# Kernel tuning notes

Hardware: AMD Instinct MI355X
Metric: run time of the kernel (lower is better)

The kernel has to match this reference:

```python
import jax, jax.numpy as jnp
import numpy as np
from jax import lax

V, E, H, M, B, L = 4000, 256, 256, 128, 32, 4
PUNC, ENG, NUM, EOS = 0, 1, 2, 3
LOGINF = 1000000.0


def _lstm(xs, h0, c0, Wih, Whh, bih, bhh):
    # xs: [T, N, H]; single-layer torch LSTM, gate order i,f,g,o
    def step(carry, x):
        h, c = carry
        g = x @ Wih.T + bih + h @ Whh.T + bhh
        i, f, gg, o = jnp.split(g, 4, axis=-1)
        c = jax.nn.sigmoid(f) * c + jax.nn.sigmoid(i) * jnp.tanh(gg)
        h = jax.nn.sigmoid(o) * jnp.tanh(c)
        return (h, c), h
    _, hs = lax.scan(step, (h0, c0), xs)
    return hs


def _forward(x, lengths, embedding, e2v_b, enc_Wih, enc_Whh, enc_bih, enc_bhh,
             enc_h0, enc_c0, dec_Wih, dec_Whh, dec_bih, dec_bhh,
             dht_W, dht_b, sos_W, sos_b):
    xT = x.T  # [M, B]
    inputs = embedding[xT]  # [M, B, H]
    is_single = ((xT == PUNC) | (xT == ENG) | (xT == NUM)).astype(jnp.float32) * (-LOGINF)  # [M, B]

    # context encoder (learned init states broadcast over batch), output halved
    h0 = jnp.broadcast_to(enc_h0, (B, H))
    c0 = jnp.broadcast_to(enc_c0, (B, H))
    enc_out = _lstm(inputs, h0, c0, enc_Wih, enc_Whh, enc_bih, enc_bhh) * 0.5  # [M, B, H]

    S = M - 2
    starts = jnp.arange(1, M - 1)  # [S] segment start positions
    enc_prev = enc_out[starts - 1]  # [S, B, H]
    sos = enc_prev @ sos_W.T + sos_b                       # start-of-segment symbol [S,B,H]
    dec_h0 = jnp.tanh(enc_prev @ dht_W.T + dht_b)          # decoder h init (1 layer) [S,B,H]
    dec_c0 = jnp.zeros_like(dec_h0)

    pad_in = jnp.concatenate([inputs, jnp.zeros((L, B, H), inputs.dtype)], axis=0)  # [M+L,B,H]
    idx = starts[:, None] + jnp.arange(L)[None, :]  # [S, L] token positions j_start+t
    seg_in = pad_in[idx]  # [S, L, B, H]
    dec_in = jnp.concatenate([sos[:, None], seg_in], axis=1)  # [S, L+1, B, H]
    dec_in = dec_in.transpose(1, 0, 2, 3).reshape(L + 1, S * B, H)
    dec_out = _lstm(dec_in, dec_h0.reshape(S * B, H), dec_c0.reshape(S * B, H),
                    dec_Wih, dec_Whh, dec_bih, dec_bhh).reshape(L + 1, S, B, H)

    logits = jnp.einsum('tsbh,vh->tsbv', dec_out, embedding) + e2v_b  # tied e2v weight
    logp = jax.nn.log_softmax(logits, axis=-1)  # [L+1, S, B, V]

    x_pad = jnp.concatenate([xT, jnp.zeros((L, B), xT.dtype)], axis=0)
    tgt = x_pad[idx]  # [S, L, B]
    lp_t = logp[:L].transpose(1, 0, 2, 3)  # [S, L, B, V]
    tlp = jnp.take_along_axis(lp_t, tgt[..., None].astype(jnp.int32), axis=-1)[..., 0]  # [S,L,B]

    is_pad = jnp.concatenate([is_single, jnp.zeros((L, B), jnp.float32)], axis=0)
    seg_is = is_pad[idx]  # is_single[j_start+t], [S,L,B]
    kge1 = (jnp.arange(L) >= 1).astype(jnp.float32)[None, :, None]  # t>=1 mask
    cum = jnp.cumsum(tlp + seg_is * kge1, axis=1)
    cum = cum + kge1 * is_single[starts][:, None, :]  # add is_single[j_start] once from k==1 on

    eos_lp = logp[1:, :, :, EOS].transpose(1, 0, 2)  # [S, L, B]
    logpy_seg = cum + eos_lp
    j_len = jnp.minimum(L, (M - 1) - starts)  # [S]
    kvalid = jnp.arange(L)[None, :] < j_len[:, None]
    logpy_seg = jnp.where(kvalid[:, :, None], logpy_seg, -LOGINF)

    row0 = jnp.full((1, L, B), -LOGINF, jnp.float32).at[0, 0].set(0.0)
    logpy = jnp.concatenate([row0, logpy_seg], axis=0)  # [M-1, L, B]

    # seg_lp[e, d-1] = logpy[j_start+1 = e-(d-1)][d-1] for segment length d ending at e
    e_idx = jnp.arange(M - 1)[:, None] - jnp.arange(L)[None, :]  # [M-1, L]
    gathered = logpy[jnp.clip(e_idx, 0, M - 2), jnp.arange(L)[None, :]]  # [M-1, L, B]
    seg_lp = jnp.where((e_idx >= 1)[:, :, None], gathered, -LOGINF)

    def dp_step(buf, lp_e):  # buf[d-1] = alpha[e-d], [L, B]
        a = jax.scipy.special.logsumexp(buf + lp_e, axis=0)  # [B]
        return jnp.concatenate([a[None], buf[:-1]], axis=0), a

    buf0 = jnp.full((L, B), -LOGINF, jnp.float32).at[0].set(0.0)  # alpha[0]=0
    _, alphas_rest = lax.scan(dp_step, buf0, seg_lp[1:])  # e = 1..M-2
    alphas = jnp.concatenate([jnp.zeros((1, B), jnp.float32), alphas_rest], axis=0)  # [M-1, B]

    nll = -alphas[lengths - 2, jnp.arange(B)]
    total = jnp.sum(lengths) - 2 * B
    return jnp.sum(nll) / total.astype(jnp.float32)


def setup_inputs() -> dict:
    key = jax.random.key(0)
    ks = jax.random.split(key, 16)
    w = lambda k, shape: (jax.random.normal(k, shape, jnp.float32) * 0.05)
    return {
        'x': jax.random.randint(ks[0], (B, M), 0, V, jnp.int32),
        'lengths': jnp.full((B,), M, jnp.int32),
        'embedding': jax.random.uniform(ks[1], (V, E), jnp.float32, -1.0, 1.0),
        'e2v_b': w(ks[2], (V,)),
        'enc_Wih': w(ks[3], (4 * H, H)),
        'enc_Whh': w(ks[4], (4 * H, H)),
        'enc_bih': w(ks[5], (4 * H,)),
        'enc_bhh': w(ks[6], (4 * H,)),
        'enc_h0': jnp.zeros((1, H), jnp.float32),
        'enc_c0': jnp.zeros((1, H), jnp.float32),
        'dec_Wih': w(ks[7], (4 * H, H)),
        'dec_Whh': w(ks[8], (4 * H, H)),
        'dec_bih': w(ks[9], (4 * H,)),
        'dec_bhh': w(ks[10], (4 * H,)),
        'dht_W': w(ks[11], (H, H)),
        'dht_b': w(ks[12], (H,)),
        'sos_W': w(ks[13], (H, H)),
        'sos_b': w(ks[14], (H,)),
    }


def reference(x, lengths, embedding, e2v_b, enc_Wih, enc_Whh, enc_bih, enc_bhh,
              enc_h0, enc_c0, dec_Wih, dec_Whh, dec_bih, dec_bhh,
              dht_W, dht_b, sos_W, sos_b):
    return _forward(x, lengths, embedding, e2v_b, enc_Wih, enc_Whh, enc_bih, enc_bhh,
                    enc_h0, enc_c0, dec_Wih, dec_Whh, dec_bih, dec_bhh,
                    dht_W, dht_b, sos_W, sos_b)
```

## Files before the change

kernel.cpp:

```cpp
#include <hip/hip_runtime.h>
#include <math.h>


#define LOGNEG -1000000.0f
#define GF_BIAS 1
#define GF_TANH 2
#define GF_F16OUT 16
#define ZSHIFT 8.0f

typedef unsigned int uint32;
typedef _Float16 half2_t __attribute__((ext_vector_type(2)));
typedef _Float16 half8_t __attribute__((ext_vector_type(8)));
typedef float    f32x4_t __attribute__((ext_vector_type(4)));

__device__ __forceinline__ float sigmf_(float x){ return 1.0f/(1.0f+expf(-x)); }

__device__ __forceinline__ float dot2f(uint32 w, uint32 h, float acc){
#if __has_builtin(__builtin_amdgcn_fdot2)
    return __builtin_amdgcn_fdot2(__builtin_bit_cast(half2_t, w),
                                  __builtin_bit_cast(half2_t, h), acc, false);
#else
    half2_t a = __builtin_bit_cast(half2_t, w);
    half2_t b = __builtin_bit_cast(half2_t, h);
    return acc + (float)a[0]*(float)b[0] + (float)a[1]*(float)b[1];
#endif
}

__device__ __forceinline__ void gemm16_body(
    _Float16* Bs, int tid,
    const _Float16* __restrict__ A, const _Float16* __restrict__ W,
    const float* __restrict__ bias, float* __restrict__ C,
    _Float16* __restrict__ C16, int N, int flags, int rowBlk, int colBlk)
{
    int wave = tid >> 6, lane = tid & 63;
    int ln = lane & 15, quad = lane >> 4;
    half8_t a[8];
    if (tid < 256){
        #pragma unroll
        for (int i = 0; i < 8; i++){
            int idx = i*256 + tid;
            int row = idx >> 5, c16 = idx & 31;
            *(uint4*)&Bs[row*264 + c16*8] =
                *(const uint4*)(W + (size_t)(colBlk+row)*256 + c16*8);
        }
        const half8_t* Ap = (const half8_t*)(A + (size_t)(rowBlk + wave*16 + ln)*256 + quad*8);
        #pragma unroll
        for (int ks = 0; ks < 8; ks++) a[ks] = Ap[ks*4];
    }
    __syncthreads();
    if (tid < 256){
        #pragma unroll
        for (int ct = 0; ct < 4; ct++){
            f32x4_t c4 = {0.f,0.f,0.f,0.f};
            const _Float16* bp = &Bs[(ct*16+ln)*264 + quad*8];
            #pragma unroll
            for (int ks = 0; ks < 8; ks++){
                half8_t b = *(const half8_t*)(bp + ks*32);
                c4 = __builtin_amdgcn_mfma_f32_16x16x32_f16(a[ks], b, c4, 0, 0, 0);
            }
            int c = colBlk + ct*16 + ln;
            #pragma unroll
            for (int reg = 0; reg < 4; reg++){
                int r = rowBlk + wave*16 + quad*4 + reg;
                float v = c4[reg];
                if (flags & GF_BIAS) v += bias[c];
                if (flags & GF_TANH) v = tanhf(v);
                if (flags & GF_F16OUT) C16[(size_t)r*N + c] = (_Float16)v;
                else                   C  [(size_t)r*N + c] = v;
            }
        }
    }
}

__global__ __launch_bounds__(256) void k_prep(
    const int* __restrict__ x,
    const float* __restrict__ emb, const float* __restrict__ e2v_b,
    const float* __restrict__ eWih, const float* __restrict__ dWih,
    const float* __restrict__ dWhh, const float* __restrict__ eWhh,
    const float* __restrict__ sosW, const float* __restrict__ dhtW,
    const float* __restrict__ ebih, const float* __restrict__ ebhh,
    const float* __restrict__ dbih, const float* __restrict__ dbhh,
    _Float16* __restrict__ emb16, float* __restrict__ biasOff,
    _Float16* __restrict__ dWih16, _Float16* __restrict__ dWhh16,
    _Float16* __restrict__ eWhh16, _Float16* __restrict__ sosW16,
    _Float16* __restrict__ dhtW16, float* __restrict__ bias_d,
    _Float16* __restrict__ emb_in16, float* __restrict__ is_s,
    _Float16* __restrict__ XgE16)
{
    __shared__ _Float16 Bs[64*264];
    int bx = blockIdx.x, tid = threadIdx.x;
    if (bx < 1465){
        #pragma unroll 1
        for (int rr = 0; rr < 8; rr++){
            int v = bx*8 + rr;
            if (v >= 11716) break;
            if (v < 4032){
                int row = v;
                emb16[(size_t)row*256 + tid] = (row < 4000) ? (_Float16)emb[(size_t)row*256 + tid] : (_Float16)0.0f;
                if (tid == 0) biasOff[row] = (row < 4000) ? (e2v_b[row] - ZSHIFT) : -200.0f;
            } else if (v < 5056){
                int r = v - 4032; dWih16[(size_t)r*256 + tid] = (_Float16)dWih[(size_t)r*256 + tid];
            } else if (v < 6080){
                int r = v - 5056; dWhh16[(size_t)r*256 + tid] = (_Float16)dWhh[(size_t)r*256 + tid];
            } else if (v < 7104){
                int r = v - 6080; eWhh16[(size_t)r*256 + tid] = (_Float16)eWhh[(size_t)r*256 + tid];
            } else if (v < 7360){
                int r = v - 7104; sosW16[(size_t)r*256 + tid] = (_Float16)sosW[(size_t)r*256 + tid];
            } else if (v < 7616){
                int r = v - 7360; dhtW16[(size_t)r*256 + tid] = (_Float16)dhtW[(size_t)r*256 + tid];
            } else if (v < 7620){
                int j = (v - 7616)*256 + tid;
                if (j < 1024) bias_d[j] = dbih[j] + dbhh[j];
            } else {
                int ri = v - 7620;
                int m = ri >> 5, b = ri & 31;
                int tok = x[b*128 + m];
                emb_in16[(size_t)ri*256 + tid] = (_Float16)emb[(size_t)tok*256 + tid];
                if (tid == 0) is_s[ri] = (tok <= 2) ? LOGNEG : 0.0f;
            }
        }
    } else {
        int tile = bx - 1465;
        int rowBlk = (tile >> 4)*64, colBlk = (tile & 15)*64;
        #pragma unroll
        for (int i = 0; i < 8; i++){
            int idx = i*256 + tid;
            int row = idx >> 5, c16 = idx & 31;
            const float* src = eWih + (size_t)(colBlk+row)*256 + c16*8;
            float4 f0 = *(const float4*)src;
            float4 f1 = *(const float4*)(src + 4);
            half8_t hv;
            hv[0]=(_Float16)f0.x; hv[1]=(_Float16)f0.y; hv[2]=(_Float16)f0.z; hv[3]=(_Float16)f0.w;
            hv[4]=(_Float16)f1.x; hv[5]=(_Float16)f1.y; hv[6]=(_Float16)f1.z; hv[7]=(_Float16)f1.w;
            *(half8_t*)&Bs[row*264 + c16*8] = hv;
        }
        int wave = tid >> 6, lane = tid & 63;
        int ln = lane & 15, quad = lane >> 4;
        int r = rowBlk + wave*16 + ln;
        int m = r >> 5, b_ = r & 31;
        int tok = x[b_*128 + m];
        half8_t a[8];
        #pragma unroll
        for (int ks = 0; ks < 8; ks++){
            const float* ap = emb + (size_t)tok*256 + quad*8 + ks*32;
            float4 f0 = *(const float4*)ap;
            float4 f1 = *(const float4*)(ap + 4);
            half8_t hv;
            hv[0]=(_Float16)f0.x; hv[1]=(_Float16)f0.y; hv[2]=(_Float16)f0.z; hv[3]=(_Float16)f0.w;
            hv[4]=(_Float16)f1.x; hv[5]=(_Float16)f1.y; hv[6]=(_Float16)f1.z; hv[7]=(_Float16)f1.w;
            a[ks] = hv;
        }
        __syncthreads();
        #pragma unroll
        for (int ct = 0; ct < 4; ct++){
            f32x4_t c4 = {0.f,0.f,0.f,0.f};
            const _Float16* bp = &Bs[(ct*16+ln)*264 + quad*8];
            #pragma unroll
            for (int ks = 0; ks < 8; ks++){
                half8_t b = *(const half8_t*)(bp + ks*32);
                c4 = __builtin_amdgcn_mfma_f32_16x16x32_f16(a[ks], b, c4, 0, 0, 0);
            }
            int c = colBlk + ct*16 + ln;
            float bb = ebih[c] + ebhh[c];
            #pragma unroll
            for (int reg = 0; reg < 4; reg++){
                int rr2 = rowBlk + wave*16 + quad*4 + reg;
                XgE16[(size_t)rr2*1024 + c] = (_Float16)(c4[reg] + bb);
            }
        }
    }
}

__global__ void __attribute__((amdgpu_flat_work_group_size(512,512), amdgpu_waves_per_eu(2,2)))
k_enc_rnn(
    const _Float16* __restrict__ Xg16, const _Float16* __restrict__ Whh16,
    const float* __restrict__ h0, const float* __restrict__ c0,
    _Float16* __restrict__ enc_out16,
    const _Float16* __restrict__ emb_in16, const _Float16* __restrict__ dWih16,
    const float* __restrict__ bias_d, _Float16* __restrict__ Xg16dec)
{
    extern __shared__ char smem[];
    const int bx = blockIdx.x, tid = threadIdx.x;
    if (bx >= 32){
        int eng = tid >> 8, ltid = tid & 255;
        _Float16* Bs = (_Float16*)smem + (size_t)eng*(64*264);
        int base = (bx - 32)*2 + eng;
        for (int rnd = 0; rnd < 3; rnd++){
            int tile = rnd*448 + base;
            __syncthreads();
            if (tile < 1024)
                gemm16_body(Bs, ltid, emb_in16, dWih16, bias_d, nullptr, Xg16dec,
                            1024, GF_BIAS|GF_F16OUT, (tile >> 4)*64, (tile & 15)*64);
            else
                __syncthreads();
        }
        return;
    }
    uint4*     wlds = (uint4*)smem;
    _Float16*  hb   = (_Float16*)(smem + 147456);
    const int b = bx;
    const int w_ = tid >> 6, l_ = tid & 63;
    const int u  = w_*32 + (l_ & 31);
    const int hi = l_ >> 5;
    const int rA = hi*512 + u;
    const int rB = rA + 256;

    const uint4* pA = (const uint4*)(Whh16 + (size_t)rA*256);
    const uint4* pB = (const uint4*)(Whh16 + (size_t)rB*256);
    uint4 wA[23], wB[23];
    #pragma unroll
    for (int i = 0; i < 23; i++){ wA[i] = pA[i]; wB[i] = pB[i]; }
    #pragma unroll
    for (int i = 0; i < 9; i++){
        wlds[(i*2 + 0)*512 + tid] = pA[23 + i];
        wlds[(i*2 + 1)*512 + tid] = pB[23 + i];
    }
    float c = c0[u];
    if (tid < 256) hb[tid] = (_Float16)h0[tid];
    __syncthreads();

    float xgA = (float)Xg16[(size_t)b*1024 + rA];
    float xgB = (float)Xg16[(size_t)b*1024 + rB];

    for (int t = 0; t < 128; t++){
        const int cur = t & 1, nxt = cur ^ 1;
        float nxgA = 0.f, nxgB = 0.f;
        if (t < 127){
            const _Float16* xp = Xg16 + ((size_t)((t+1)*32 + b))*1024;
            nxgA = (float)xp[rA]; nxgB = (float)xp[rB];
        }
        const uint4* hu4 = (const uint4*)(hb + cur*256);
        float aA = 0.f, aB = 0.f;
        #pragma unroll
        for (int i = 0; i < 23; i++){
            uint4 hh = hu4[i];
            aA = dot2f(wA[i].x, hh.x, aA); aA = dot2f(wA[i].y, hh.y, aA);
            aA = dot2f(wA[i].z, hh.z, aA); aA = dot2f(wA[i].w, hh.w, aA);
            aB = dot2f(wB[i].x, hh.x, aB); aB = dot2f(wB[i].y, hh.y, aB);
            aB = dot2f(wB[i].z, hh.z, aB); aB = dot2f(wB[i].w, hh.w, aB);
        }
        #pragma unroll
        for (int i = 0; i < 9; i++){
            uint4 hh = hu4[23 + i];
            uint4 vA = wlds[(i*2 + 0)*512 + tid];
            uint4 vB = wlds[(i*2 + 1)*512 + tid];
            aA = dot2f(vA.x, hh.x, aA); aA = dot2f(vA.y, hh.y, aA);
            aA = dot2f(vA.z, hh.z, aA); aA = dot2f(vA.w, hh.w, aA);
            aB = dot2f(vB.x, hh.x, aB); aB = dot2f(vB.y, hh.y, aB);
            aB = dot2f(vB.z, hh.z, aB); aB = dot2f(vB.w, hh.w, aB);
        }
        float gA = aA + xgA, gB = aB + xgB;
        float oA = __shfl_xor(gA, 32, 64);
        float oB = __shfl_xor(gB, 32, 64);
        float gi = hi ? oA : gA;
        float gf = hi ? oB : gB;
        float gg = hi ? gA : oA;
        float go = hi ? gB : oB;
        c = sigmf_(gf)*c + sigmf_(gi)*tanhf(gg);
        float hn = sigmf_(go)*tanhf(c);
        if (!hi){
            enc_out16[((size_t)(t*32 + b))*256 + u] = (_Float16)(0.5f*hn);
            hb[nxt*256 + u] = (_Float16)hn;
        }
        __syncthreads();
        xgA = nxgA; xgB = nxgB;
    }
}

__global__ __launch_bounds__(256) void k_head(
    const _Float16* __restrict__ enc_out16,
    const _Float16* __restrict__ sosW16, const float* __restrict__ sos_b, _Float16* __restrict__ sos16,
    const _Float16* __restrict__ dhtW16, const float* __restrict__ dht_b, _Float16* __restrict__ dech0_16)
{
    __shared__ _Float16 Bs[64*264];
    int z = blockIdx.z;
    gemm16_body(Bs, threadIdx.x, enc_out16,
                z ? dhtW16 : sosW16, z ? dht_b : sos_b, nullptr,
                z ? dech0_16 : sos16, 256,
                z ? (GF_BIAS|GF_TANH|GF_F16OUT) : (GF_BIAS|GF_F16OUT),
                blockIdx.y*64, blockIdx.x*64);
}

__global__ __launch_bounds__(256) void k_dec_step(
    const _Float16* __restrict__ hprev, const _Float16* __restrict__ sosA,
    const _Float16* __restrict__ dWhh16, const _Float16* __restrict__ dWih16,
    const _Float16* __restrict__ base16, const float* __restrict__ bias_d,
    float* __restrict__ dec_c, _Float16* __restrict__ dec16_j, int jstep)
{
    __shared__ _Float16 Bs[64*264];
    int tid = threadIdx.x;
    int wave = tid >> 6, lane = tid & 63;
    int ln = lane & 15, quad = lane >> 4;
    int u0 = blockIdx.x * 64, r0 = blockIdx.y * 64;

    half8_t aH[8], aS[8];
    {
        const half8_t* Ap = (const half8_t*)(hprev + (size_t)(r0 + wave*16 + ln)*256 + quad*8);
        #pragma unroll
        for (int ks = 0; ks < 8; ks++) aH[ks] = Ap[ks*4];
    }
    if (jstep == 0){
        const half8_t* Ap = (const half8_t*)(sosA + (size_t)(r0 + wave*16 + ln)*256 + quad*8);
        #pragma unroll
        for (int ks = 0; ks < 8; ks++) aS[ks] = Ap[ks*4];
    }

    f32x4_t cg[4][4];
    #pragma unroll
    for (int g = 0; g < 4; g++){
        int colBlk = g*256 + u0;
        __syncthreads();
        #pragma unroll
        for (int i = 0; i < 8; i++){
            int idx = i*256 + tid;
            int row = idx >> 5, c16 = idx & 31;
            *(uint4*)&Bs[row*264 + c16*8] =
                *(const uint4*)(dWhh16 + (size_t)(colBlk+row)*256 + c16*8);
        }
        __syncthreads();
        #pragma unroll
        for (int ct = 0; ct < 4; ct++){
            f32x4_t c4 = {0.f,0.f,0.f,0.f};
            const _Float16* bp = &Bs[(ct*16+ln)*264 + quad*8];
            #pragma unroll
            for (int ks = 0; ks < 8; ks++){
                half8_t b = *(const half8_t*)(bp + ks*32);
                c4 = __builtin_amdgcn_mfma_f32_16x16x32_f16(aH[ks], b, c4, 0, 0, 0);
            }
            cg[g][ct] = c4;
        }
        if (jstep == 0){
            __syncthreads();
            #pragma unroll
            for (int i = 0; i < 8; i++){
                int idx = i*256 + tid;
                int row = idx >> 5, c16 = idx & 31;
                *(uint4*)&Bs[row*264 + c16*8] =
                    *(const uint4*)(dWih16 + (size_t)(colBlk+row)*256 + c16*8);
            }
            __syncthreads();
            #pragma unroll
            for (int ct = 0; ct < 4; ct++){
                f32x4_t c4 = cg[g][ct];
                const _Float16* bp = &Bs[(ct*16+ln)*264 + quad*8];
                #pragma unroll
                for (int ks = 0; ks < 8; ks++){
                    half8_t b = *(const half8_t*)(bp + ks*32);
                    c4 = __builtin_amdgcn_mfma_f32_16x16x32_f16(aS[ks], b, c4, 0, 0, 0);
                }
                cg[g][ct] = c4;
            }
        }
    }
    #pragma unroll
    for (int ct = 0; ct < 4; ct++){
        int u = u0 + ct*16 + ln;
        #pragma unroll
        for (int reg = 0; reg < 4; reg++){
            int r = r0 + wave*16 + quad*4 + reg;
            float bi, bf, bg, bo;
            if (jstep == 0){
                bi = bias_d[u]; bf = bias_d[256+u]; bg = bias_d[512+u]; bo = bias_d[768+u];
            } else {
                int s = r >> 5, b_ = r & 31;
                int m = s + jstep;
                if (m < 128){
                    const _Float16* bp2 = base16 + (size_t)(m*32+b_)*1024 + u;
                    bi = (float)bp2[0]; bf = (float)bp2[256]; bg = (float)bp2[512]; bo = (float)bp2[768];
                } else {
                    bi = bias_d[u]; bf = bias_d[256+u]; bg = bias_d[512+u]; bo = bias_d[768+u];
                }
            }
            float gi = cg[0][ct][reg] + bi;
            float gf = cg[1][ct][reg] + bf;
            float gg = cg[2][ct][reg] + bg;
            float go = cg[3][ct][reg] + bo;
            float cv = (jstep == 0) ? 0.0f : dec_c[(size_t)r*256 + u];
            cv = sigmf_(gf)*cv + sigmf_(gi)*tanhf(gg);
            float hv = sigmf_(go)*tanhf(cv);
            dec_c[(size_t)r*256 + u] = cv;
            dec16_j[(size_t)r*256 + u] = (_Float16)hv;
        }
    }
}

__global__ __launch_bounds__(256) void k_logits(
    const _Float16* __restrict__ dec16, const _Float16* __restrict__ emb16,
    const float* __restrict__ biasOff, const int* __restrict__ x,
    float* __restrict__ ps, float* __restrict__ pzt, float* __restrict__ pze)
{
    __shared__ _Float16 Bs[64*264];
    __shared__ int tgt_s[128];
    int tid = threadIdx.x;
    int wave = tid >> 6, lane = tid & 63;
    int ln = lane & 15, quad = lane >> 4;
    int r0 = blockIdx.x * 128;
    int q = blockIdx.y;
    int vt0 = q*16, vt1 = (q == 3) ? 63 : (vt0 + 16);

    if (tid < 128){
        int r = r0 + tid;
        if (r >= 20160) r = 20159;
        int t = r / 4032, sb = r % 4032;
        int s_ = sb >> 5, b = sb & 31;
        int m = s_ + 1 + t;
        tgt_s[tid] = (m < 128) ? x[b*128 + m] : 0;
    }
    half8_t aA[8], aB[8];
    {
        int ra = r0 + wave*16 + ln;        if (ra >= 20160) ra = 20159;
        int rb = r0 + 64 + wave*16 + ln;   if (rb >= 20160) rb = 20159;
        const half8_t* Ap = (const half8_t*)(dec16 + (size_t)ra*256 + quad*8);
        const half8_t* Bp = (const half8_t*)(dec16 + (size_t)rb*256 + quad*8);
        #pragma unroll
        for (int ks = 0; ks < 8; ks++){ aA[ks] = Ap[ks*4]; aB[ks] = Bp[ks*4]; }
    }
    __syncthreads();
    int tgA[4], tgB[4];
    #pragma unroll
    for (int reg = 0; reg < 4; reg++){
        tgA[reg] = tgt_s[wave*16 + quad*4 + reg];
        tgB[reg] = tgt_s[64 + wave*16 + quad*4 + reg];
    }

    float sA[4] = {0.f,0.f,0.f,0.f}, sB[4] = {0.f,0.f,0.f,0.f};
    float ztA[4] = {-1e30f,-1e30f,-1e30f,-1e30f}, ztB[4] = {-1e30f,-1e30f,-1e30f,-1e30f};
    float zeA[4] = {-1e30f,-1e30f,-1e30f,-1e30f}, zeB[4] = {-1e30f,-1e30f,-1e30f,-1e30f};

    for (int vt = vt0; vt < vt1; vt++){
        int v0 = vt*64;
        __syncthreads();
        #pragma unroll
        for (int i = 0; i < 8; i++){
            int idx = i*256 + tid;
            int row = idx >> 5, c16 = idx & 31;
            *(uint4*)&Bs[row*264 + c16*8] =
                *(const uint4*)(emb16 + (size_t)(v0+row)*256 + c16*8);
        }
        __syncthreads();

        #pragma unroll
        for (int ct = 0; ct < 4; ct++){
            f32x4_t cA = {0.f,0.f,0.f,0.f}, cB = {0.f,0.f,0.f,0.f};
            const _Float16* bp = &Bs[(ct*16+ln)*264 + quad*8];
            #pragma unroll
            for (int ks = 0; ks < 8; ks++){
                half8_t b = *(const half8_t*)(bp + ks*32);
                cA = __builtin_amdgcn_mfma_f32_16x16x32_f16(aA[ks], b, cA, 0, 0, 0);
                cB = __builtin_amdgcn_mfma_f32_16x16x32_f16(aB[ks], b, cB, 0, 0, 0);
            }
            int vv = v0 + ct*16 + ln;
            float bb = biasOff[vv];
            #pragma unroll
            for (int reg = 0; reg < 4; reg++){
                float zA = cA[reg] + bb, zB = cB[reg] + bb;
                sA[reg] += __expf(zA);
                sB[reg] += __expf(zB);
                if (vv == tgA[reg]) ztA[reg] = zA;
                if (vv == tgB[reg]) ztB[reg] = zB;
                if (vv == 3){ zeA[reg] = zA; zeB[reg] = zB; }
            }
        }
    }
    #pragma unroll
    for (int reg = 0; reg < 4; reg++){
        float vsA = sA[reg], vtA = ztA[reg], veA = zeA[reg];
        float vsB = sB[reg], vtB = ztB[reg], veB = zeB[reg];
        #pragma unroll
        for (int off = 1; off < 16; off <<= 1){
            vsA += __shfl_xor(vsA, off, 64);
            vsB += __shfl_xor(vsB, off, 64);
            vtA = fmaxf(vtA, __shfl_xor(vtA, off, 64));
            vtB = fmaxf(vtB, __shfl_xor(vtB, off, 64));
            veA = fmaxf(veA, __shfl_xor(veA, off, 64));
            veB = fmaxf(veB, __shfl_xor(veB, off, 64));
        }
        if (ln == 0){
            int rA = r0 + wave*16 + quad*4 + reg;
            int rB = rA + 64;
            if (rA < 20160){ ps[q*20160+rA] = vsA; pzt[q*20160+rA] = vtA; pze[q*20160+rA] = veA; }
            if (rB < 20160){ ps[q*20160+rB] = vsB; pzt[q*20160+rB] = vtB; pze[q*20160+rB] = veB; }
        }
    }
}

__global__ __launch_bounds__(256) void k_comb_fin(
    const float* __restrict__ ps, const float* __restrict__ pzt,
    const float* __restrict__ pze, const int* __restrict__ x,
    const float* __restrict__ is_s, const int* __restrict__ lengths,
    float* __restrict__ tlp, float* __restrict__ eosb,
    float* __restrict__ seg_g, float* __restrict__ out,
    unsigned int* __restrict__ counter)
{
    int tid = threadIdx.x;
    int r = blockIdx.x*256 + tid;
    if (r < 20160){
        float lse = __logf(ps[r] + ps[20160+r] + ps[2*20160+r] + ps[3*20160+r]);
        int t = r / 4032, sb = r % 4032;
        int s_ = sb >> 5, b = sb & 31;
        int m = s_ + 1 + t;
        int tg = (m < 128) ? x[b*128 + m] : 0;
        float zt = pzt[(tg >> 10)*20160 + r];
        float ze = pze[r];
        if (t < 4)  tlp[(t*126+s_)*32 + b]      = zt - lse;
        if (t >= 1) eosb[((t-1)*126+s_)*32 + b] = ze - lse;
    }
    __threadfence();
    __syncthreads();
    __shared__ int lastBlk;
    if (tid == 0){
        unsigned old = __hip_atomic_fetch_add(counter, 1u, __ATOMIC_ACQ_REL,
                                              __HIP_MEMORY_SCOPE_AGENT);
        lastBlk = (old == 78) ? 1 : 0;
    }
    __syncthreads();
    if (!lastBlk) return;
    __threadfence();

    int k = tid >> 5, b = tid & 31;
    if (tid < 128){
        for (int s = 0; s < 126; s++){
            float cum = 0.f;
            for (int kk = 0; kk <= k; kk++) cum += tlp[(kk*126+s)*32 + b];
            if (k >= 1){
                for (int kk = 1; kk <= k; kk++){
                    int m = s+1+kk;
                    if (m < 128) cum += is_s[m*32+b];
                }
                cum += is_s[(s+1)*32 + b];
            }
            float lp = cum + eosb[(k*126+s)*32 + b];
            int jl = min(4, 126 - s);
            if (k >= jl) lp = LOGNEG;
            seg_g[(s*4+k)*32 + b] = lp;
        }
    }
    __threadfence_block();
    __syncthreads();
    __shared__ float nll_s[32];
    if (tid < 32){
        int target = lengths[tid] - 2;
        float b0 = 0.f, b1 = LOGNEG, b2 = LOGNEG, b3 = LOGNEG;
        float nllb = 0.f;
        for (int e = 1; e <= 126; e++){
            float v0 = b0 + seg_g[((e-1)*4+0)*32 + tid];
            float v1 = b1 + ((e >= 2) ? seg_g[((e-2)*4+1)*32 + tid] : LOGNEG);
            float v2 = b2 + ((e >= 3) ? seg_g[((e-3)*4+2)*32 + tid] : LOGNEG);
            float v3 = b3 + ((e >= 4) ? seg_g[((e-4)*4+3)*32 + tid] : LOGNEG);
            float mx = fmaxf(fmaxf(v0,v1), fmaxf(v2,v3));
            float a = mx + logf(expf(v0-mx)+expf(v1-mx)+expf(v2-mx)+expf(v3-mx));
            if (e == target) nllb = -a;
            b3 = b2; b2 = b1; b1 = b0; b0 = a;
        }
        nll_s[tid] = nllb;
    }
    __syncthreads();
    if (tid == 0){
        float tot = 0.f; int lsum = 0;
        for (int i = 0; i < 32; i++){ tot += nll_s[i]; lsum += lengths[i]; }
        out[0] = tot / (float)(lsum - 64);
    }
}

extern "C" void kernel_launch(void* const* d_in, const int* in_sizes, int n_in,
                              void* d_out, int out_size, void* d_ws, size_t ws_size,
                              hipStream_t stream)
{
    const int*   x        = (const int*)  d_in[0];
    const int*   lengths  = (const int*)  d_in[1];
    const float* emb      = (const float*)d_in[2];
    const float* e2v_b    = (const float*)d_in[3];
    const float* enc_Wih  = (const float*)d_in[4];
    const float* enc_Whh  = (const float*)d_in[5];
    const float* enc_bih  = (const float*)d_in[6];
    const float* enc_bhh  = (const float*)d_in[7];
    const float* enc_h0   = (const float*)d_in[8];
    const float* enc_c0   = (const float*)d_in[9];
    const float* dec_Wih  = (const float*)d_in[10];
    const float* dec_Whh  = (const float*)d_in[11];
    const float* dec_bih  = (const float*)d_in[12];
    const float* dec_bhh  = (const float*)d_in[13];
    const float* dht_W    = (const float*)d_in[14];
    const float* dht_b    = (const float*)d_in[15];
    const float* sos_W    = (const float*)d_in[16];
    const float* sos_b    = (const float*)d_in[17];
    float* out = (float*)d_out;

    char* wsb = (char*)d_ws;
    size_t off = 0;
    auto alloc = [&](size_t bytes)->void*{
        void* p = (void*)(wsb + off);
        off += ((bytes + 255)/256)*256;
        return p;
    };
    _Float16* emb16    = (_Float16*)alloc((size_t)4032*256*2);
    _Float16* dWih16   = (_Float16*)alloc((size_t)1024*256*2);
    _Float16* dWhh16   = (_Float16*)alloc((size_t)1024*256*2);
    _Float16* eWhh16   = (_Float16*)alloc((size_t)1024*256*2);
    _Float16* sosW16   = (_Float16*)alloc((size_t)256*256*2);
    _Float16* dhtW16   = (_Float16*)alloc((size_t)256*256*2);
    _Float16* emb_in16 = (_Float16*)alloc((size_t)4096*256*2);
    _Float16* XgE16    = (_Float16*)alloc((size_t)4096*1024*2);
    _Float16* Xgdec16  = (_Float16*)alloc((size_t)4096*1024*2);
    _Float16* enc_out16= (_Float16*)alloc((size_t)4096*256*2);
    _Float16* sos16    = (_Float16*)alloc((size_t)4032*256*2);
    _Float16* dech0_16 = (_Float16*)alloc((size_t)4032*256*2);
    _Float16* dec16    = (_Float16*)alloc((size_t)5*4032*256*2);
    float*    dec_c    = (float*)alloc((size_t)4032*256*4);
    float*    biasOff  = (float*)alloc(4032*4);
    float*    bias_d   = (float*)alloc(1024*4);
    float*    is_s     = (float*)alloc(4096*4);
    float*    ps       = (float*)alloc((size_t)4*20160*4);
    float*    pzt      = (float*)alloc((size_t)4*20160*4);
    float*    pze      = (float*)alloc((size_t)4*20160*4);
    float*    tlp      = (float*)alloc((size_t)4*126*32*4);
    float*    eosb     = (float*)alloc((size_t)4*126*32*4);
    float*    seg_g    = (float*)alloc((size_t)126*4*32*4);
    unsigned int* counter = (unsigned int*)alloc(256);
    (void)ws_size; (void)in_sizes; (void)n_in; (void)out_size;

    hipFuncSetAttribute(reinterpret_cast<const void*>(k_enc_rnn),
                        hipFuncAttributeMaxDynamicSharedMemorySize, 148480);

    hipMemsetAsync(counter, 0, sizeof(unsigned int), stream);
    k_prep<<<2489, 256, 0, stream>>>(x, emb, e2v_b, enc_Wih, dec_Wih, dec_Whh, enc_Whh,
        sos_W, dht_W, enc_bih, enc_bhh, dec_bih, dec_bhh,
        emb16, biasOff, dWih16, dWhh16, eWhh16, sosW16, dhtW16, bias_d,
        emb_in16, is_s, XgE16);
    k_enc_rnn<<<256, 512, 148480, stream>>>(XgE16, eWhh16, enc_h0, enc_c0, enc_out16,
        emb_in16, dWih16, bias_d, Xgdec16);
    k_head<<<dim3(4,63,2), 256, 0, stream>>>(enc_out16, sosW16, sos_b, sos16,
        dhtW16, dht_b, dech0_16);
    for (int j = 0; j < 5; j++){
        const _Float16* hA = (j == 0) ? dech0_16 : (dec16 + (size_t)(j-1)*4032*256);
        k_dec_step<<<dim3(4,63), 256, 0, stream>>>(hA, sos16, dWhh16, dWih16,
            Xgdec16, bias_d, dec_c, dec16 + (size_t)j*4032*256, j);
    }
    k_logits<<<dim3(158,4), 256, 0, stream>>>(dec16, emb16, biasOff, x, ps, pzt, pze);
    k_comb_fin<<<79, 256, 0, stream>>>(ps, pzt, pze, x, is_s, lengths,
        tlp, eosb, seg_g, out, counter);
}
```

Before: 819.0 us.

## Fuse head, decoder steps, logits and combine into one persistent kernel

Replaces the head GEMM, five decoder-step launches, the logits kernel and the combine kernel with a single persistent kernel of 256 blocks × 512 threads. Each block runs two 256-thread sub-engines, and a software global barrier separates the stages. This removes several kernel launches and their gaps. In exchange, every stage is limited to 512 task slots per round, and the barrier spins on atomics. All blocks must be co-resident or the barrier deadlocks.

```diff
diff --git a/kernel.cpp b/kernel.cpp
--- a/kernel.cpp
+++ b/kernel.cpp
@@ -24,6 +24,23 @@
     half2_t b = __builtin_bit_cast(half2_t, h);
     return acc + (float)a[0]*(float)b[0] + (float)a[1]*(float)b[1];
 #endif
+}
+
+__device__ __forceinline__ void gbar(unsigned* cnt, unsigned* gen, int nblk){
+    __syncthreads();
+    __threadfence();
+    if (threadIdx.x == 0){
+        unsigned g0 = __hip_atomic_load(gen, __ATOMIC_ACQUIRE, __HIP_MEMORY_SCOPE_AGENT);
+        unsigned old = __hip_atomic_fetch_add(cnt, 1u, __ATOMIC_ACQ_REL, __HIP_MEMORY_SCOPE_AGENT);
+        if (old == (unsigned)(nblk - 1)){
+            __hip_atomic_store(cnt, 0u, __ATOMIC_RELAXED, __HIP_MEMORY_SCOPE_AGENT);
+            __hip_atomic_fetch_add(gen, 1u, __ATOMIC_ACQ_REL, __HIP_MEMORY_SCOPE_AGENT);
+        } else {
+            while (__hip_atomic_load(gen, __ATOMIC_ACQUIRE, __HIP_MEMORY_SCOPE_AGENT) == g0)
+                __builtin_amdgcn_s_sleep(2);
+        }
+    }
+    __syncthreads();
 }
 
 __device__ __forceinline__ void gemm16_body(
@@ -267,42 +284,27 @@
     }
 }
 
-__global__ __launch_bounds__(256) void k_head(
-    const _Float16* __restrict__ enc_out16,
-    const _Float16* __restrict__ sosW16, const float* __restrict__ sos_b, _Float16* __restrict__ sos16,
-    const _Float16* __restrict__ dhtW16, const float* __restrict__ dht_b, _Float16* __restrict__ dech0_16)
-{
-    __shared__ _Float16 Bs[64*264];
-    int z = blockIdx.z;
-    gemm16_body(Bs, threadIdx.x, enc_out16,
-                z ? dhtW16 : sosW16, z ? dht_b : sos_b, nullptr,
-                z ? dech0_16 : sos16, 256,
-                z ? (GF_BIAS|GF_TANH|GF_F16OUT) : (GF_BIAS|GF_F16OUT),
-                blockIdx.y*64, blockIdx.x*64);
-}
-
-__global__ __launch_bounds__(256) void k_dec_step(
+__device__ __forceinline__ void dec_body(
+    bool act, _Float16* Bs, int tid,
     const _Float16* __restrict__ hprev, const _Float16* __restrict__ sosA,
     const _Float16* __restrict__ dWhh16, const _Float16* __restrict__ dWih16,
     const _Float16* __restrict__ base16, const float* __restrict__ bias_d,
-    float* __restrict__ dec_c, _Float16* __restrict__ dec16_j, int jstep)
+    float* __restrict__ dec_c, _Float16* __restrict__ dec16_j,
+    int jstep, int u0, int r0)
 {
-    __shared__ _Float16 Bs[64*264];
-    int tid = threadIdx.x;
     int wave = tid >> 6, lane = tid & 63;
     int ln = lane & 15, quad = lane >> 4;
-    int u0 = blockIdx.x * 64, r0 = blockIdx.y * 64;
 
     half8_t aH[8], aS[8];
-    {
+    if (act){
         const half8_t* Ap = (const half8_t*)(hprev + (size_t)(r0 + wave*16 + ln)*256 + quad*8);
         #pragma unroll
         for (int ks = 0; ks < 8; ks++) aH[ks] = Ap[ks*4];
-    }
-    if (jstep == 0){
-        const half8_t* Ap = (const half8_t*)(sosA + (size_t)(r0 + wave*16 + ln)*256 + quad*8);
-        #pragma unroll
-        for (int ks = 0; ks < 8; ks++) aS[ks] = Ap[ks*4];
+        if (jstep == 0){
+            const half8_t* Ap2 = (const half8_t*)(sosA + (size_t)(r0 + wave*16 + ln)*256 + quad*8);
+            #pragma unroll
+            for (int ks = 0; ks < 8; ks++) aS[ks] = Ap2[ks*4];
+        }
     }
 
     f32x4_t cg[4][4];
@@ -310,95 +312,102 @@
     for (int g = 0; g < 4; g++){
         int colBlk = g*256 + u0;
         __syncthreads();
-        #pragma unroll
-        for (int i = 0; i < 8; i++){
-            int idx = i*256 + tid;
-            int row = idx >> 5, c16 = idx & 31;
-            *(uint4*)&Bs[row*264 + c16*8] =
-                *(const uint4*)(dWhh16 + (size_t)(colBlk+row)*256 + c16*8);
-        }
-        __syncthreads();
-        #pragma unroll
-        for (int ct = 0; ct < 4; ct++){
-            f32x4_t c4 = {0.f,0.f,0.f,0.f};
-            const _Float16* bp = &Bs[(ct*16+ln)*264 + quad*8];
-            #pragma unroll
-            for (int ks = 0; ks < 8; ks++){
-                half8_t b = *(const half8_t*)(bp + ks*32);
-                c4 = __builtin_amdgcn_mfma_f32_16x16x32_f16(aH[ks], b, c4, 0, 0, 0);
-            }
-            cg[g][ct] = c4;
-        }
-        if (jstep == 0){
-            __syncthreads();
+        if (act){
             #pragma unroll
             for (int i = 0; i < 8; i++){
                 int idx = i*256 + tid;
                 int row = idx >> 5, c16 = idx & 31;
                 *(uint4*)&Bs[row*264 + c16*8] =
-                    *(const uint4*)(dWih16 + (size_t)(colBlk+row)*256 + c16*8);
-            }
-            __syncthreads();
+                    *(const uint4*)(dWhh16 + (size_t)(colBlk+row)*256 + c16*8);
+            }
+        }
+        __syncthreads();
+        if (act){
             #pragma unroll
             for (int ct = 0; ct < 4; ct++){
-                f32x4_t c4 = cg[g][ct];
+                f32x4_t c4 = {0.f,0.f,0.f,0.f};
                 const _Float16* bp = &Bs[(ct*16+ln)*264 + quad*8];
                 #pragma unroll
                 for (int ks = 0; ks < 8; ks++){
                     half8_t b = *(const half8_t*)(bp + ks*32);
-                    c4 = __builtin_amdgcn_mfma_f32_16x16x32_f16(aS[ks], b, c4, 0, 0, 0);
+                    c4 = __builtin_amdgcn_mfma_f32_16x16x32_f16(aH[ks], b, c4, 0, 0, 0);
                 }
                 cg[g][ct] = c4;
             }
         }
-    }
-    #pragma unroll
-    for (int ct = 0; ct < 4; ct++){
-        int u = u0 + ct*16 + ln;
-        #pragma unroll
-        for (int reg = 0; reg < 4; reg++){
-            int r = r0 + wave*16 + quad*4 + reg;
-            float bi, bf, bg, bo;
-            if (jstep == 0){
-                bi = bias_d[u]; bf = bias_d[256+u]; bg = bias_d[512+u]; bo = bias_d[768+u];
-            } else {
-                int s = r >> 5, b_ = r & 31;
-                int m = s + jstep;
-                if (m < 128){
-                    const _Float16* bp2 = base16 + (size_t)(m*32+b_)*1024 + u;
-                    bi = (float)bp2[0]; bf = (float)bp2[256]; bg = (float)bp2[512]; bo = (float)bp2[768];
+        if (jstep == 0){
+            __syncthreads();
+            if (act){
+                #pragma unroll
+                for (int i = 0; i < 8; i++){
+                    int idx = i*256 + tid;
+                    int row = idx >> 5, c16 = idx & 31;
+                    *(uint4*)&Bs[row*264 + c16*8] =
+                        *(const uint4*)(dWih16 + (size_t)(colBlk+row)*256 + c16*8);
+                }
+            }
+            __syncthreads();
+            if (act){
+                #pragma unroll
+                for (int ct = 0; ct < 4; ct++){
+                    f32x4_t c4 = cg[g][ct];
+                    const _Float16* bp = &Bs[(ct*16+ln)*264 + quad*8];
+                    #pragma unroll
+                    for (int ks = 0; ks < 8; ks++){
+                        half8_t b = *(const half8_t*)(bp + ks*32);
+                        c4 = __builtin_amdgcn_mfma_f32_16x16x32_f16(aS[ks], b, c4, 0, 0, 0);
+                    }
+                    cg[g][ct] = c4;
+                }
+            }
+        }
+    }
+    if (act){
+        #pragma unroll
+        for (int ct = 0; ct < 4; ct++){
+            int u = u0 + ct*16 + ln;
+            #pragma unroll
+            for (int reg = 0; reg < 4; reg++){
+                int r = r0 + wave*16 + quad*4 + reg;
+                float bi, bf, bg, bo;
+                if (jstep == 0){
+                    bi = bias_d[u]; bf = bias_d[256+u]; bg = bias_d[512+u]; bo = bias_d[768+u];
                 } else {
-                    bi = bias_d[u]; bf = bias_d[256+u]; bg = bias_d[512+u]; bo = bias_d[768+u];
+                    int s = r >> 5, b_ = r & 31;
+                    int m = s + jstep;
+                    if (m < 128){
+                        const _Float16* bp2 = base16 + (size_t)(m*32+b_)*1024 + u;
+                        bi = (float)bp2[0]; bf = (float)bp2[256]; bg = (float)bp2[512]; bo = (float)bp2[768];
+                    } else {
+                        bi = bias_d[u]; bf = bias_d[256+u]; bg = bias_d[512+u]; bo = bias_d[768+u];
+                    }
                 }
-            }
-            float gi = cg[0][ct][reg] + bi;
-            float gf = cg[1][ct][reg] + bf;
-            float gg = cg[2][ct][reg] + bg;
-            float go = cg[3][ct][reg] + bo;
-            float cv = (jstep == 0) ? 0.0f : dec_c[(size_t)r*256 + u];
-            cv = sigmf_(gf)*cv + sigmf_(gi)*tanhf(gg);
-            float hv = sigmf_(go)*tanhf(cv);
-            dec_c[(size_t)r*256 + u] = cv;
-            dec16_j[(size_t)r*256 + u] = (_Float16)hv;
-        }
-    }
-}
-
-__global__ __launch_bounds__(256) void k_logits(
+                float gi = cg[0][ct][reg] + bi;
+                float gf = cg[1][ct][reg] + bf;
+                float gg = cg[2][ct][reg] + bg;
+                float go = cg[3][ct][reg] + bo;
+                float cv = (jstep == 0) ? 0.0f : dec_c[(size_t)r*256 + u];
+                cv = sigmf_(gf)*cv + sigmf_(gi)*tanhf(gg);
+                float hv = sigmf_(go)*tanhf(cv);
+                dec_c[(size_t)r*256 + u] = cv;
+                dec16_j[(size_t)r*256 + u] = (_Float16)hv;
+            }
+        }
+    }
+}
+
+__device__ __forceinline__ void logits_body(
+    bool act, _Float16* Bs, int* tgt_s, int tid,
     const _Float16* __restrict__ dec16, const _Float16* __restrict__ emb16,
     const float* __restrict__ biasOff, const int* __restrict__ x,
-    float* __restrict__ ps, float* __restrict__ pzt, float* __restrict__ pze)
+    float* __restrict__ ps, float* __restrict__ pzt, float* __restrict__ pze,
+    int r0, int q)
 {
-    __shared__ _Float16 Bs[64*264];
-    __shared__ int tgt_s[128];
-    int tid = threadIdx.x;
     int wave = tid >> 6, lane = tid & 63;
     int ln = lane & 15, quad = lane >> 4;
-    int r0 = blockIdx.x * 128;
-    int q = blockIdx.y;
     int vt0 = q*16, vt1 = (q == 3) ? 63 : (vt0 + 16);
 
-    if (tid < 128){
+    if (act && tid < 128){
         int r = r0 + tid;
         if (r >= 20160) r = 20159;
         int t = r / 4032, sb = r % 4032;
@@ -407,7 +416,7 @@
         tgt_s[tid] = (m < 128) ? x[b*128 + m] : 0;
     }
     half8_t aA[8], aB[8];
-    {
+    if (act){
         int ra = r0 + wave*16 + ln;        if (ra >= 20160) ra = 20159;
         int rb = r0 + 64 + wave*16 + ln;   if (rb >= 20160) rb = 20159;
         const half8_t* Ap = (const half8_t*)(dec16 + (size_t)ra*256 + quad*8);
@@ -417,106 +426,155 @@
     }
     __syncthreads();
     int tgA[4], tgB[4];
-    #pragma unroll
-    for (int reg = 0; reg < 4; reg++){
-        tgA[reg] = tgt_s[wave*16 + quad*4 + reg];
-        tgB[reg] = tgt_s[64 + wave*16 + quad*4 + reg];
+    if (act){
+        #pragma unroll
+        for (int reg = 0; reg < 4; reg++){
+            tgA[reg] = tgt_s[wave*16 + quad*4 + reg];
+            tgB[reg] = tgt_s[64 + wave*16 + quad*4 + reg];
+        }
     }
 
     float sA[4] = {0.f,0.f,0.f,0.f}, sB[4] = {0.f,0.f,0.f,0.f};
     float ztA[4] = {-1e30f,-1e30f,-1e30f,-1e30f}, ztB[4] = {-1e30f,-1e30f,-1e30f,-1e30f};
     float zeA[4] = {-1e30f,-1e30f,-1e30f,-1e30f}, zeB[4] = {-1e30f,-1e30f,-1e30f,-1e30f};
 
-    for (int vt = vt0; vt < vt1; vt++){
+    for (int k = 0; k < 16; k++){
+        int vt = vt0 + k;
+        bool a2 = act && (vt < vt1);
         int v0 = vt*64;
         __syncthreads();
-        #pragma unroll
-        for (int i = 0; i < 8; i++){
-            int idx = i*256 + tid;
-            int row = idx >> 5, c16 = idx & 31;
-            *(uint4*)&Bs[row*264 + c16*8] =
-                *(const uint4*)(emb16 + (size_t)(v0+row)*256 + c16*8);
+        if (a2){
+            #pragma unroll
+            for (int i = 0; i < 8; i++){
+                int idx = i*256 + tid;
+                int row = idx >> 5, c16 = idx & 31;
+                *(uint4*)&Bs[row*264 + c16*8] =
+                    *(const uint4*)(emb16 + (size_t)(v0+row)*256 + c16*8);
+            }
         }
         __syncthreads();
-
-        #pragma unroll
-        for (int ct = 0; ct < 4; ct++){
-            f32x4_t cA = {0.f,0.f,0.f,0.f}, cB = {0.f,0.f,0.f,0.f};
-            const _Float16* bp = &Bs[(ct*16+ln)*264 + quad*8];
-            #pragma unroll
-            for (int ks = 0; ks < 8; ks++){
-                half8_t b = *(const half8_t*)(bp + ks*32);
-                cA = __builtin_amdgcn_mfma_f32_16x16x32_f16(aA[ks], b, cA, 0, 0, 0);
-                cB = __builtin_amdgcn_mfma_f32_16x16x32_f16(aB[ks], b, cB, 0, 0, 0);
-            }
-            int vv = v0 + ct*16 + ln;
-            float bb = biasOff[vv];
-            #pragma unroll
-            for (int reg = 0; reg < 4; reg++){
-                float zA = cA[reg] + bb, zB = cB[reg] + bb;
-                sA[reg] += __expf(zA);
-                sB[reg] += __expf(zB);
-                if (vv == tgA[reg]) ztA[reg] = zA;
-                if (vv == tgB[reg]) ztB[reg] = zB;
-                if (vv == 3){ zeA[reg] = zA; zeB[reg] = zB; }
-            }
-        }
-    }
-    #pragma unroll
-    for (int reg = 0; reg < 4; reg++){
-        float vsA = sA[reg], vtA = ztA[reg], veA = zeA[reg];
-        float vsB = sB[reg], vtB = ztB[reg], veB = zeB[reg];
-        #pragma unroll
-        for (int off = 1; off < 16; off <<= 1){
-            vsA += __shfl_xor(vsA, off, 64);
-            vsB += __shfl_xor(vsB, off, 64);
-            vtA = fmaxf(vtA, __shfl_xor(vtA, off, 64));
-            vtB = fmaxf(vtB, __shfl_xor(vtB, off, 64));
-            veA = fmaxf(veA, __shfl_xor(veA, off, 64));
-            veB = fmaxf(veB, __shfl_xor(veB, off, 64));
-        }
-        if (ln == 0){
-            int rA = r0 + wave*16 + quad*4 + reg;
-            int rB = rA + 64;
-            if (rA < 20160){ ps[q*20160+rA] = vsA; pzt[q*20160+rA] = vtA; pze[q*20160+rA] = veA; }
-            if (rB < 20160){ ps[q*20160+rB] = vsB; pzt[q*20160+rB] = vtB; pze[q*20160+rB] = veB; }
-        }
-    }
-}
-
-__global__ __launch_bounds__(256) void k_comb_fin(
-    const float* __restrict__ ps, const float* __restrict__ pzt,
-    const float* __restrict__ pze, const int* __restrict__ x,
+        if (a2){
+            #pragma unroll
+            for (int ct = 0; ct < 4; ct++){
+                f32x4_t cA = {0.f,0.f,0.f,0.f}, cB = {0.f,0.f,0.f,0.f};
+                const _Float16* bp = &Bs[(ct*16+ln)*264 + quad*8];
+                #pragma unroll
+                for (int ks = 0; ks < 8; ks++){
+                    half8_t b = *(const half8_t*)(bp + ks*32);
+                    cA = __builtin_amdgcn_mfma_f32_16x16x32_f16(aA[ks], b, cA, 0, 0, 0);
+                    cB = __builtin_amdgcn_mfma_f32_16x16x32_f16(aB[ks], b, cB, 0, 0, 0);
+                }
+                int vv = v0 + ct*16 + ln;
+                float bb = biasOff[vv];
+                #pragma unroll
+                for (int reg = 0; reg < 4; reg++){
+                    float zA = cA[reg] + bb, zB = cB[reg] + bb;
+                    sA[reg] += __expf(zA);
+                    sB[reg] += __expf(zB);
+                    if (vv == tgA[reg]) ztA[reg] = zA;
+                    if (vv == tgB[reg]) ztB[reg] = zB;
+                    if (vv == 3){ zeA[reg] = zA; zeB[reg] = zB; }
+                }
+            }
+        }
+    }
+    if (act){
+        #pragma unroll
+        for (int reg = 0; reg < 4; reg++){
+            float vsA = sA[reg], vtA = ztA[reg], veA = zeA[reg];
+            float vsB = sB[reg], vtB = ztB[reg], veB = zeB[reg];
+            #pragma unroll
+            for (int off = 1; off < 16; off <<= 1){
+                vsA += __shfl_xor(vsA, off, 64);
+                vsB += __shfl_xor(vsB, off, 64);
+                vtA = fmaxf(vtA, __shfl_xor(vtA, off, 64));
+                vtB = fmaxf(vtB, __shfl_xor(vtB, off, 64));
+                veA = fmaxf(veA, __shfl_xor(veA, off, 64));
+                veB = fmaxf(veB, __shfl_xor(veB, off, 64));
+            }
+            if (ln == 0){
+                int rA = r0 + wave*16 + quad*4 + reg;
+                int rB = rA + 64;
+                if (rA < 20160){ ps[q*20160+rA] = vsA; pzt[q*20160+rA] = vtA; pze[q*20160+rA] = veA; }
+                if (rB < 20160){ ps[q*20160+rB] = vsB; pzt[q*20160+rB] = vtB; pze[q*20160+rB] = veB; }
+            }
+        }
+    }
+}
+
+__global__ void __attribute__((amdgpu_flat_work_group_size(512,512)))
+k_post(
+    const _Float16* __restrict__ enc_out16,
+    const _Float16* __restrict__ sosW16, const float* __restrict__ sos_b, _Float16* __restrict__ sos16,
+    const _Float16* __restrict__ dhtW16, const float* __restrict__ dht_b, _Float16* __restrict__ dech0_16,
+    const _Float16* __restrict__ dWhh16, const _Float16* __restrict__ dWih16,
+    const _Float16* __restrict__ Xgdec16, const float* __restrict__ bias_d,
+    float* __restrict__ dec_c, _Float16* __restrict__ dec16,
+    const _Float16* __restrict__ emb16, const float* __restrict__ biasOff,
+    const int* __restrict__ x,
+    float* __restrict__ ps, float* __restrict__ pzt, float* __restrict__ pze,
     const float* __restrict__ is_s, const int* __restrict__ lengths,
     float* __restrict__ tlp, float* __restrict__ eosb,
     float* __restrict__ seg_g, float* __restrict__ out,
-    unsigned int* __restrict__ counter)
+    unsigned* __restrict__ bar)
 {
-    int tid = threadIdx.x;
-    int r = blockIdx.x*256 + tid;
-    if (r < 20160){
-        float lse = __logf(ps[r] + ps[20160+r] + ps[2*20160+r] + ps[3*20160+r]);
-        int t = r / 4032, sb = r % 4032;
-        int s_ = sb >> 5, b = sb & 31;
-        int m = s_ + 1 + t;
-        int tg = (m < 128) ? x[b*128 + m] : 0;
-        float zt = pzt[(tg >> 10)*20160 + r];
-        float ze = pze[r];
-        if (t < 4)  tlp[(t*126+s_)*32 + b]      = zt - lse;
-        if (t >= 1) eosb[((t-1)*126+s_)*32 + b] = ze - lse;
-    }
-    __threadfence();
-    __syncthreads();
-    __shared__ int lastBlk;
-    if (tid == 0){
-        unsigned old = __hip_atomic_fetch_add(counter, 1u, __ATOMIC_ACQ_REL,
-                                              __HIP_MEMORY_SCOPE_AGENT);
-        lastBlk = (old == 78) ? 1 : 0;
-    }
-    __syncthreads();
-    if (!lastBlk) return;
-    __threadfence();
-
+    extern __shared__ char smem[];
+    const int bid = blockIdx.x, tid = threadIdx.x;
+    const int eng = tid >> 8, ltid = tid & 255;
+    _Float16* Bs    = (_Float16*)(smem + (size_t)eng*(64*264*2));
+    int*      tgt_s = (int*)(smem + 2*(64*264*2)) + eng*128;
+    unsigned* cnt = bar; unsigned* gen = bar + 1;
+
+    {
+        int task = bid*2 + eng;
+        if (task < 504){
+            int z = task / 252, rem = task % 252;
+            gemm16_body(Bs, ltid, enc_out16,
+                        z ? dhtW16 : sosW16, z ? dht_b : sos_b, nullptr,
+                        z ? dech0_16 : sos16, 256,
+                        z ? (GF_BIAS|GF_TANH|GF_F16OUT) : (GF_BIAS|GF_F16OUT),
+                        (rem >> 2)*64, (rem & 3)*64);
+        } else __syncthreads();
+    }
+    gbar(cnt, gen, 256);
+
+    for (int j = 0; j < 5; j++){
+        const _Float16* hA = (j == 0) ? dech0_16 : (dec16 + (size_t)(j-1)*4032*256);
+        int task = bid*2 + eng;
+        bool act = task < 252;
+        dec_body(act, Bs, ltid, hA, sos16, dWhh16, dWih16, Xgdec16, bias_d,
+                 dec_c, dec16 + (size_t)j*4032*256, j,
+                 (task & 3)*64, (task >> 2)*64);
+        gbar(cnt, gen, 256);
+    }
+
+    for (int rnd = 0; rnd < 2; rnd++){
+        int task = rnd*512 + bid*2 + eng;
+        bool act = task < 632;
+        int q  = act ? (task / 158) : 3;
+        int r0 = act ? (task % 158)*128 : 0;
+        logits_body(act, Bs, tgt_s, ltid, dec16, emb16, biasOff, x,
+                    ps, pzt, pze, r0, q);
+    }
+    gbar(cnt, gen, 256);
+
+    {
+        int r = bid*512 + tid;
+        if (r < 20160){
+            float lse = __logf(ps[r] + ps[20160+r] + ps[2*20160+r] + ps[3*20160+r]);
+            int t = r / 4032, sb = r % 4032;
+            int s_ = sb >> 5, b = sb & 31;
+            int m = s_ + 1 + t;
+            int tg = (m < 128) ? x[b*128 + m] : 0;
+            float zt = pzt[(tg >> 10)*20160 + r];
+            float ze = pze[r];
+            if (t < 4)  tlp[(t*126+s_)*32 + b]      = zt - lse;
+            if (t >= 1) eosb[((t-1)*126+s_)*32 + b] = ze - lse;
+        }
+    }
+    gbar(cnt, gen, 256);
+
+    if (bid != 0) return;
     int k = tid >> 5, b = tid & 31;
     if (tid < 128){
         for (int s = 0; s < 126; s++){
@@ -621,22 +679,19 @@
 
     hipFuncSetAttribute(reinterpret_cast<const void*>(k_enc_rnn),
                         hipFuncAttributeMaxDynamicSharedMemorySize, 148480);
-
-    hipMemsetAsync(counter, 0, sizeof(unsigned int), stream);
+    hipFuncSetAttribute(reinterpret_cast<const void*>(k_post),
+                        hipFuncAttributeMaxDynamicSharedMemorySize, 68608);
+
+    hipMemsetAsync(counter, 0, 256, stream);
     k_prep<<<2489, 256, 0, stream>>>(x, emb, e2v_b, enc_Wih, dec_Wih, dec_Whh, enc_Whh,
         sos_W, dht_W, enc_bih, enc_bhh, dec_bih, dec_bhh,
         emb16, biasOff, dWih16, dWhh16, eWhh16, sosW16, dhtW16, bias_d,
         emb_in16, is_s, XgE16);
     k_enc_rnn<<<256, 512, 148480, stream>>>(XgE16, eWhh16, enc_h0, enc_c0, enc_out16,
         emb_in16, dWih16, bias_d, Xgdec16);
-    k_head<<<dim3(4,63,2), 256, 0, stream>>>(enc_out16, sosW16, sos_b, sos16,
-        dhtW16, dht_b, dech0_16);
-    for (int j = 0; j < 5; j++){
-        const _Float16* hA = (j == 0) ? dech0_16 : (dec16 + (size_t)(j-1)*4032*256);
-        k_dec_step<<<dim3(4,63), 256, 0, stream>>>(hA, sos16, dWhh16, dWih16,
-            Xgdec16, bias_d, dec_c, dec16 + (size_t)j*4032*256, j);
-    }
-    k_logits<<<dim3(158,4), 256, 0, stream>>>(dec16, emb16, biasOff, x, ps, pzt, pze);
-    k_comb_fin<<<79, 256, 0, stream>>>(ps, pzt, pze, x, is_s, lengths,
+    k_post<<<256, 512, 68608, stream>>>(enc_out16,
+        sosW16, sos_b, sos16, dhtW16, dht_b, dech0_16,
+        dWhh16, dWih16, Xgdec16, bias_d, dec_c, dec16,
+        emb16, biasOff, x, ps, pzt, pze, is_s, lengths,
         tlp, eosb, seg_g, out, counter);
 }
```

Result: slower. 1.771 ms (+116.2%).
